# Performance work log

Hardware: AMD Instinct MI355X
Metric: run time of the kernel (lower is better)

The kernel has to match this reference:

```python
import jax, jax.numpy as jnp
import numpy as np

N_NODES = 50000
N_EDGES = 640000
HIDDEN = 128
N_LAYERS = 4
NUM_RBF = 50
CUTOFF = 4.0
N_GRAPHS = 64
VOCAB = 128
LN_EPS = 1e-5


def setup_inputs() -> dict:
    key = jax.random.key(0)
    ks = jax.random.split(key, 16)
    s = 1.0 / np.sqrt(HIDDEN)
    sr = 1.0 / np.sqrt(NUM_RBF)
    inp = {
        "x": jax.random.randint(ks[0], (N_NODES,), 0, VOCAB, dtype=jnp.int64) if jax.config.jax_enable_x64 else jax.random.randint(ks[0], (N_NODES,), 0, VOCAB).astype(jnp.int32),
        "edge_index": jax.random.randint(ks[1], (2, N_EDGES), 0, N_NODES).astype(jnp.int32),
        "edge_attr": jax.random.uniform(ks[2], (N_EDGES,), dtype=jnp.float32) * CUTOFF,
        "batch": jnp.sort(jax.random.randint(ks[3], (N_NODES,), 0, N_GRAPHS)).astype(jnp.int32),
        # embedding table
        "emb": jax.random.normal(ks[4], (VOCAB, HIDDEN), dtype=jnp.float32),
        # filter net: Linear(num_rbf, H) -> ReLU -> Linear(H, H), stacked over layers
        "fw1": jax.random.normal(ks[5], (N_LAYERS, NUM_RBF, HIDDEN), dtype=jnp.float32) * sr,
        "fb1": jnp.zeros((N_LAYERS, HIDDEN), dtype=jnp.float32),
        "fw2": jax.random.normal(ks[6], (N_LAYERS, HIDDEN, HIDDEN), dtype=jnp.float32) * s,
        "fb2": jnp.zeros((N_LAYERS, HIDDEN), dtype=jnp.float32),
        # lin: Linear(H, H) per layer
        "lw": jax.random.normal(ks[7], (N_LAYERS, HIDDEN, HIDDEN), dtype=jnp.float32) * s,
        "lb": jnp.zeros((N_LAYERS, HIDDEN), dtype=jnp.float32),
        # LayerNorm params per layer
        "ln_g": jnp.ones((N_LAYERS, HIDDEN), dtype=jnp.float32),
        "ln_b": jnp.zeros((N_LAYERS, HIDDEN), dtype=jnp.float32),
    }
    return inp


def _gaussian_smearing(dist):
    offset = jnp.linspace(0.0, CUTOFF, NUM_RBF, dtype=jnp.float32)  # [R]
    coeff = -0.5 / (CUTOFF / (NUM_RBF - 1)) ** 2
    d = dist[:, None] - offset[None, :]  # [E, R]
    return jnp.exp(coeff * d * d)


def _layer_norm(h, g, b):
    mu = jnp.mean(h, axis=-1, keepdims=True)
    var = jnp.mean(jnp.square(h - mu), axis=-1, keepdims=True)
    return (h - mu) * jax.lax.rsqrt(var + LN_EPS) * g + b


def reference(x, edge_index, edge_attr, batch, emb, fw1, fb1, fw2, fb2, lw, lb, ln_g, ln_b):
    edge_rbf = _gaussian_smearing(edge_attr)          # [E, R]
    h = emb[x]                                        # [N, H]
    row, col = edge_index[0], edge_index[1]
    for i in range(N_LAYERS):
        # FilterNet(RBF): [E, H]
        w = jax.nn.relu(edge_rbf @ fw1[i] + fb1[i]) @ fw2[i] + fb2[i]
        xl = h @ lw[i] + lb[i]                        # [N, H]
        msg = xl[col] * w                             # gather + elementwise, [E, H]
        out = jax.ops.segment_sum(msg, row, num_segments=N_NODES)
        h = _layer_norm(h + out, ln_g[i], ln_b[i])
    # global mean pool over graphs
    sums = jax.ops.segment_sum(h, batch, num_segments=N_GRAPHS)      # [G, H]
    cnt = jax.ops.segment_sum(jnp.ones((N_NODES,), h.dtype), batch, num_segments=N_GRAPHS)
    return sums / jnp.maximum(cnt, 1.0)[:, None]
```

## Files before the change

### kernel.cpp

```cpp
#include <hip/hip_runtime.h>
#include <hip/hip_bf16.h>

#define N_NODES 50000
#define N_EDGES 640000
#define HIDDEN 128
#define N_LAYERS 4
#define NUM_RBF 50
#define CUTOFF 4.0f
#define N_GRAPHS 64
#define TAB 8192
#define TG 8
#define PSPLIT 16
#define COLBITS 17
#define CMASK ((1u << COLBITS) - 1)
#define NBUCK 196
#define CHUNK 4096
#define PADMETA 990208
#define DUMMY ((uint)N_NODES)

typedef unsigned int uint;
typedef unsigned short ushort;
typedef __attribute__((ext_vector_type(8))) short bf16x8;
typedef __attribute__((ext_vector_type(4))) float f32x4;

__device__ inline ushort f2bf(float f) {
    uint u = __float_as_uint(f);
    uint r = (u + 0x7fffu + ((u >> 16) & 1u)) >> 16;
    return (ushort)r;
}
__device__ inline uint packbf(float lo, float hi) {
    return (uint)f2bf(lo) | ((uint)f2bf(hi) << 16);
}
__device__ inline float bflo(uint u) { return __uint_as_float(u << 16); }
__device__ inline float bfhi(uint u) { return __uint_as_float(u & 0xffff0000u); }

__global__ __launch_bounds__(128) void k_tab1(const float* __restrict__ fw1,
                                              const float* __restrict__ fb1,
                                              ushort* __restrict__ hidbf) {
    int bid = blockIdx.x;
    int layer = bid / (TAB / TG);
    int g0 = (bid % (TAB / TG)) * TG;
    int j = threadIdx.x;
    __shared__ float rbf[TG][NUM_RBF];
    for (int idx = j; idx < TG * NUM_RBF; idx += 128) {
        int gg = idx / NUM_RBF, r = idx % NUM_RBF;
        float d = (CUTOFF * (g0 + gg)) / (float)(TAB - 1);
        float offset = (CUTOFF * r) / (float)(NUM_RBF - 1);
        float delta = CUTOFF / (float)(NUM_RBF - 1);
        float coeff = -0.5f / (delta * delta);
        float t = d - offset;
        rbf[gg][r] = expf(coeff * t * t);
    }
    __syncthreads();
    const float* w1 = fw1 + layer * NUM_RBF * HIDDEN;
    float b1 = fb1[layer * HIDDEN + j];
    float acc[TG];
    #pragma unroll
    for (int gg = 0; gg < TG; gg++) acc[gg] = b1;
    for (int r = 0; r < NUM_RBF; r++) {
        float w = w1[r * HIDDEN + j];
        #pragma unroll
        for (int gg = 0; gg < TG; gg++) acc[gg] = fmaf(rbf[gg][r], w, acc[gg]);
    }
    #pragma unroll
    for (int gg = 0; gg < TG; gg++)
        hidbf[((size_t)layer * TAB + g0 + gg) * HIDDEN + j] = f2bf(fmaxf(acc[gg], 0.0f));
}

__global__ __launch_bounds__(256) void k_tab2(const ushort* __restrict__ hidbf,
                                              const uint4* __restrict__ pb2,
                                              const float* __restrict__ fb2,
                                              ushort* __restrict__ ctab) {
    int wave = threadIdx.x >> 6, lane = threadIdx.x & 63;
    int m0 = (blockIdx.x * 4 + wave) * 16;
    int layer = m0 / TAB;
    int quad = lane >> 4, ml = lane & 15;
    const ushort* arow = hidbf + (size_t)(m0 + ml) * HIDDEN + quad * 8;
    bf16x8 a[4];
    #pragma unroll
    for (int kc = 0; kc < 4; kc++) a[kc] = *(const bf16x8*)(arow + kc * 32);
    const uint4* pb = pb2 + (size_t)layer * 8 * 4 * 64;
    const float* bias = fb2 + layer * HIDDEN;
    #pragma unroll
    for (int nt = 0; nt < 8; nt++) {
        f32x4 acc = {0.f, 0.f, 0.f, 0.f};
        #pragma unroll
        for (int kc = 0; kc < 4; kc++) {
            bf16x8 b = *(const bf16x8*)(pb + (nt * 4 + kc) * 64 + lane);
            acc = __builtin_amdgcn_mfma_f32_16x16x32_bf16(a[kc], b, acc, 0, 0, 0);
        }
        int col = nt * 16 + ml;
        float bv = bias[col];
        #pragma unroll
        for (int r = 0; r < 4; r++) {
            int row = m0 + quad * 4 + r;
            ctab[(size_t)row * HIDDEN + col] = f2bf(acc[r] + bv);
        }
    }
}

__global__ void k_embed(const int* __restrict__ x, const float* __restrict__ emb,
                        ushort* __restrict__ hbf) {
    int idx = blockIdx.x * 256 + threadIdx.x;
    if (idx >= N_NODES * 32) return;
    int n = idx >> 5, q = idx & 31;
    float4 v = ((const float4*)emb)[x[n] * 32 + q];
    uint2 p;
    p.x = packbf(v.x, v.y);
    p.y = packbf(v.z, v.w);
    ((uint2*)hbf)[idx] = p;
}

__global__ void k_packw(const float* __restrict__ lw, const float* __restrict__ fw2,
                        uint4* __restrict__ pb, uint4* __restrict__ pb2) {
    int idx = blockIdx.x * 256 + threadIdx.x;
    if (idx >= 2 * N_LAYERS * 8 * 4 * 64) return;
    int which = idx >> 13;
    int rem = idx & 8191;
    int lane = rem & 63;
    int kc = (rem >> 6) & 3;
    int nt = (rem >> 8) & 7;
    int layer = rem >> 11;
    int quad = lane >> 4, nl = lane & 15;
    int n = nt * 16 + nl;
    const float* w = (which ? fw2 : lw) + layer * HIDDEN * HIDDEN;
    uint r[4];
    #pragma unroll
    for (int jj = 0; jj < 4; jj++) {
        int k = kc * 32 + quad * 8 + 2 * jj;
        r[jj] = packbf(w[k * HIDDEN + n], w[(k + 1) * HIDDEN + n]);
    }
    uint4 o; o.x = r[0]; o.y = r[1]; o.z = r[2]; o.w = r[3];
    (which ? pb2 : pb)[rem] = o;
}

__global__ void k_count(const int* __restrict__ row, int* __restrict__ counts) {
    int e = blockIdx.x * 256 + threadIdx.x;
    if (e < N_EDGES) atomicAdd(&counts[row[e]], 1);
}

__global__ void k_scan1(const int* __restrict__ counts, int* __restrict__ partial,
                        int* __restrict__ blocksum) {
    int i = blockIdx.x * 256 + threadIdx.x;
    int c = (i < N_NODES) ? counts[i] : 0;
    int v = (c + 7) & ~7;
    int lane = threadIdx.x & 63;
    int wid = threadIdx.x >> 6;
    int s = v;
    #pragma unroll
    for (int off = 1; off < 64; off <<= 1) {
        int t = __shfl_up(s, off, 64);
        if (lane >= off) s += t;
    }
    __shared__ int wsum[4];
    if (lane == 63) wsum[wid] = s;
    __syncthreads();
    int woff = 0;
    for (int w = 0; w < wid; w++) woff += wsum[w];
    int incl = s + woff;
    if (i < N_NODES) partial[i] = incl - v;
    if (threadIdx.x == 255) blocksum[blockIdx.x] = incl;
}

__global__ void k_scan2(int* __restrict__ blocksum, int nblk,
                        const int* __restrict__ batch, int* __restrict__ gstart,
                        int* __restrict__ padtotal) {
    int tid = threadIdx.x;
    if (tid <= N_GRAPHS) {
        int lo = 0, hi = N_NODES;
        while (lo < hi) {
            int mid = (lo + hi) >> 1;
            if (batch[mid] < tid) lo = mid + 1; else hi = mid;
        }
        gstart[tid] = lo;
    }
    int v = (tid < nblk) ? blocksum[tid] : 0;
    int lane = tid & 63, wid = tid >> 6;
    int s = v;
    #pragma unroll
    for (int off = 1; off < 64; off <<= 1) {
        int t = __shfl_up(s, off, 64);
        if (lane >= off) s += t;
    }
    __shared__ int wsum[4];
    if (lane == 63) wsum[wid] = s;
    __syncthreads();
    int woff = 0;
    for (int w = 0; w < wid; w++) woff += wsum[w];
    int incl = s + woff;
    if (tid < nblk) blocksum[tid] = incl - v;
    if (tid == nblk - 1) *padtotal = incl;
}

__global__ void k_scan3(const int* __restrict__ partial, const int* __restrict__ blocksum,
                        const int* __restrict__ padtotal,
                        int* __restrict__ offsets, int* __restrict__ bcur) {
    int i = blockIdx.x * 256 + threadIdx.x;
    if (i < N_NODES) {
        int o = partial[i] + blocksum[blockIdx.x];
        offsets[i] = o;
        if ((i & 255) == 0) bcur[i >> 8] = o;
    }
    if (i == 0) offsets[N_NODES] = *padtotal;
}

__global__ __launch_bounds__(256) void k_bucket(const int* __restrict__ row,
                                                const int* __restrict__ col,
                                                const float* __restrict__ eattr,
                                                int* __restrict__ bcur,
                                                uint2* __restrict__ bs) {
    __shared__ uint2 stage[CHUNK];
    __shared__ int hist[256], lscan[256], lcur[256], gbase[256];
    __shared__ int wsum[4];
    int t = threadIdx.x;
    int e0 = blockIdx.x * CHUNK;
    int ne = min(CHUNK, N_EDGES - e0);
    hist[t] = 0;
    __syncthreads();
    for (int i = t; i < ne; i += 256)
        atomicAdd(&hist[row[e0 + i] >> 8], 1);
    __syncthreads();
    int v = hist[t];
    int lane = t & 63, wid = t >> 6;
    int s = v;
    #pragma unroll
    for (int off = 1; off < 64; off <<= 1) {
        int u = __shfl_up(s, off, 64);
        if (lane >= off) s += u;
    }
    if (lane == 63) wsum[wid] = s;
    __syncthreads();
    int woff = 0;
    for (int w = 0; w < wid; w++) woff += wsum[w];
    int excl = s + woff - v;
    lscan[t] = excl;
    lcur[t] = excl;
    if (v > 0) gbase[t] = atomicAdd(&bcur[t], v);
    __syncthreads();
    for (int i = t; i < ne; i += 256) {
        int e = e0 + i;
        int r = row[e];
        float tt = eattr[e] * ((float)(TAB - 1) / CUTOFF);
        int gi = (int)(tt + 0.5f);
        gi = min(max(gi, 0), TAB - 1);
        int pos = atomicAdd(&lcur[r >> 8], 1);
        uint2 sv;
        sv.x = (uint)col[e] | ((uint)gi << COLBITS);
        sv.y = (uint)r;
        stage[pos] = sv;
    }
    __syncthreads();
    for (int i = t; i < ne; i += 256) {
        uint2 sv = stage[i];
        int b = sv.y >> 8;
        bs[gbase[b] + (i - lscan[b])] = sv;
    }
}

__global__ __launch_bounds__(256) void k_scatter(const uint2* __restrict__ bs,
                                                 const int* __restrict__ offsets,
                                                 const int* __restrict__ bend,
                                                 uint* __restrict__ meta) {
    int b = blockIdx.x, t = threadIdx.x;
    int r0 = b << 8;
    __shared__ int cur[256];
    int rmax = min(r0 + 256, N_NODES);
    cur[t] = offsets[min(r0 + t, N_NODES)];
    __syncthreads();
    int s = offsets[r0], e = bend[b];
    for (int i = s + t; i < e; i += 256) {
        uint2 v = bs[i];
        int slot = atomicAdd(&cur[v.y - r0], 1);
        meta[slot] = v.x;
    }
    __syncthreads();
    int node = r0 + t;
    if (node < rmax) {
        int end = offsets[node + 1];
        for (int i = cur[t]; i < end; i++) meta[i] = DUMMY;
    }
}

__global__ __launch_bounds__(256) void k_xl(const ushort* __restrict__ hbf,
                                            const uint4* __restrict__ pb,
                                            const float* __restrict__ lb,
                                            ushort* __restrict__ xlb) {
    int wave = threadIdx.x >> 6, lane = threadIdx.x & 63;
    int m0 = (blockIdx.x * 4 + wave) * 16;
    if (m0 >= N_NODES) return;
    int quad = lane >> 4, ml = lane & 15;
    const ushort* arow = hbf + (size_t)(m0 + ml) * HIDDEN + quad * 8;
    bf16x8 a[4];
    #pragma unroll
    for (int kc = 0; kc < 4; kc++) a[kc] = *(const bf16x8*)(arow + kc * 32);
    #pragma unroll
    for (int nt = 0; nt < 8; nt++) {
        f32x4 acc = {0.f, 0.f, 0.f, 0.f};
        #pragma unroll
        for (int kc = 0; kc < 4; kc++) {
            bf16x8 b = *(const bf16x8*)(pb + (nt * 4 + kc) * 64 + lane);
            acc = __builtin_amdgcn_mfma_f32_16x16x32_bf16(a[kc], b, acc, 0, 0, 0);
        }
        int col = nt * 16 + ml;
        float bias = lb[col];
        #pragma unroll
        for (int r = 0; r < 4; r++) {
            int row = m0 + quad * 4 + r;
            xlb[(size_t)row * HIDDEN + col] = f2bf(acc[r] + bias);
        }
    }
}

__global__ __launch_bounds__(256) void k_agg(const ushort* __restrict__ xlb,
                                             const uint* __restrict__ meta,
                                             const int* __restrict__ offsets,
                                             const uint* __restrict__ ctab,
                                             const ushort* __restrict__ hb_in,
                                             const float* __restrict__ g,
                                             const float* __restrict__ b,
                                             ushort* __restrict__ hbf_out) {
    int wid = threadIdx.x >> 6;
    int lane = threadIdx.x & 63;
    int n = blockIdx.x * 4 + wid;
    if (n >= N_NODES) return;
    const uint* xl2 = (const uint*)xlb;
    float accx = 0.f, accy = 0.f;
    int p0 = offsets[n], p1 = offsets[n + 1];
    int cnt = p1 - p0;
    for (int base = 0; base < cnt; base += 64) {
        int li = p0 + base + lane;
        uint mlv = meta[min(li, PADMETA - 1)];
        int kk = min(64, cnt - base);
        int p = 0;
        for (; p + 16 <= kk; p += 16) {
            uint wA[8], xA[8], wB[8], xB[8];
            #pragma unroll
            for (int i = 0; i < 8; i++) {
                uint m = __builtin_amdgcn_readlane(mlv, p + i);
                wA[i] = ctab[(m >> COLBITS) * 64 + lane];
                xA[i] = xl2[(m & CMASK) * 64 + lane];
            }
            #pragma unroll
            for (int i = 0; i < 8; i++) {
                uint m = __builtin_amdgcn_readlane(mlv, p + 8 + i);
                wB[i] = ctab[(m >> COLBITS) * 64 + lane];
                xB[i] = xl2[(m & CMASK) * 64 + lane];
            }
            #pragma unroll
            for (int i = 0; i < 8; i++) {
                accx = fmaf(bflo(wA[i]), bflo(xA[i]), accx);
                accy = fmaf(bfhi(wA[i]), bfhi(xA[i]), accy);
            }
            #pragma unroll
            for (int i = 0; i < 8; i++) {
                accx = fmaf(bflo(wB[i]), bflo(xB[i]), accx);
                accy = fmaf(bfhi(wB[i]), bfhi(xB[i]), accy);
            }
        }
        for (; p < kk; p += 8) {
            uint wA[8], xA[8];
            #pragma unroll
            for (int i = 0; i < 8; i++) {
                uint m = __builtin_amdgcn_readlane(mlv, p + i);
                wA[i] = ctab[(m >> COLBITS) * 64 + lane];
                xA[i] = xl2[(m & CMASK) * 64 + lane];
            }
            #pragma unroll
            for (int i = 0; i < 8; i++) {
                accx = fmaf(bflo(wA[i]), bflo(xA[i]), accx);
                accy = fmaf(bfhi(wA[i]), bfhi(xA[i]), accy);
            }
        }
    }
    uint hvp = ((const uint*)hb_in)[n * 64 + lane];
    float vx = bflo(hvp) + accx, vy = bfhi(hvp) + accy;
    float s = vx + vy;
    #pragma unroll
    for (int off = 32; off; off >>= 1) s += __shfl_xor(s, off, 64);
    float mu = s * (1.0f / 128.0f);
    float dx = vx - mu, dy = vy - mu;
    float s2 = dx * dx + dy * dy;
    #pragma unroll
    for (int off = 32; off; off >>= 1) s2 += __shfl_xor(s2, off, 64);
    float rstd = rsqrtf(s2 * (1.0f / 128.0f) + 1e-5f);
    float2 gv = ((const float2*)g)[lane];
    float2 bv = ((const float2*)b)[lane];
    float ox = fmaf(dx * rstd, gv.x, bv.x);
    float oy = fmaf(dy * rstd, gv.y, bv.y);
    ((uint*)hbf_out)[n * 64 + lane] = packbf(ox, oy);
}

__global__ __launch_bounds__(256) void k_pool_part(const ushort* __restrict__ hbf,
                                                   const int* __restrict__ gstart,
                                                   float* __restrict__ partial) {
    int g = blockIdx.x / PSPLIT;
    int t = blockIdx.x % PSPLIT;
    int jp = threadIdx.x & 63;
    int half = threadIdx.x >> 6;
    int s = gstart[g], e = gstart[g + 1];
    float accx = 0.f, accy = 0.f;
    const uint* h2 = (const uint*)hbf;
    for (int n = s + t * 4 + half; n < e; n += PSPLIT * 4) {
        uint v = h2[n * 64 + jp];
        accx += bflo(v);
        accy += bfhi(v);
    }
    __shared__ float redx[256], redy[256];
    redx[threadIdx.x] = accx;
    redy[threadIdx.x] = accy;
    __syncthreads();
    if (half == 0) {
        float tx = redx[jp] + redx[jp + 64] + redx[jp + 128] + redx[jp + 192];
        float ty = redy[jp] + redy[jp + 64] + redy[jp + 128] + redy[jp + 192];
        float2 o; o.x = tx; o.y = ty;
        ((float2*)partial)[(g * PSPLIT + t) * 64 + jp] = o;
    }
}

__global__ void k_pool_fin(const float* __restrict__ partial,
                           const int* __restrict__ gstart,
                           float* __restrict__ out) {
    int idx = blockIdx.x * 128 + threadIdx.x;
    int g = idx >> 7, j = idx & 127;
    float tot = 0.f;
    #pragma unroll
    for (int t = 0; t < PSPLIT; t++) tot += partial[(g * PSPLIT + t) * HIDDEN + j];
    float c = (float)(gstart[g + 1] - gstart[g]);
    out[idx] = tot / fmaxf(c, 1.0f);
}

extern "C" void kernel_launch(void* const* d_in, const int* in_sizes, int n_in,
                              void* d_out, int out_size, void* d_ws, size_t ws_size,
                              hipStream_t stream) {
    const int* x = (const int*)d_in[0];
    const int* edge_index = (const int*)d_in[1];
    const int* row = edge_index;
    const int* col = edge_index + N_EDGES;
    const float* eattr = (const float*)d_in[2];
    const int* batch = (const int*)d_in[3];
    const float* emb = (const float*)d_in[4];
    const float* fw1 = (const float*)d_in[5];
    const float* fb1 = (const float*)d_in[6];
    const float* fw2 = (const float*)d_in[7];
    const float* fb2 = (const float*)d_in[8];
    const float* lw = (const float*)d_in[9];
    const float* lb = (const float*)d_in[10];
    const float* ln_g = (const float*)d_in[11];
    const float* ln_b = (const float*)d_in[12];
    float* out = (float*)d_out;

    char* ws = (char*)d_ws;
    size_t off = 0;
    auto alloc = [&](size_t bytes) -> void* {
        void* p = ws + off;
        off = (off + bytes + 255) & ~(size_t)255;
        return p;
    };
    uint* ctab     = (uint*)alloc((size_t)N_LAYERS * TAB * 64 * 4);
    ushort* hidbf  = (ushort*)alloc((size_t)N_LAYERS * TAB * HIDDEN * 2);
    ushort* hbf_a  = (ushort*)alloc((size_t)N_NODES * HIDDEN * 2);
    ushort* hbf_b  = (ushort*)alloc((size_t)N_NODES * HIDDEN * 2);
    ushort* xlb    = (ushort*)alloc((size_t)(N_NODES + 1) * HIDDEN * 2);
    uint4* pb      = (uint4*)alloc((size_t)N_LAYERS * 8 * 4 * 64 * 16);
    uint4* pb2     = (uint4*)alloc((size_t)N_LAYERS * 8 * 4 * 64 * 16);
    int* counts    = (int*)alloc((size_t)(N_NODES + 1) * 4);
    int* offsets   = (int*)alloc((size_t)(N_NODES + 1) * 4);
    int* partial   = (int*)alloc((size_t)N_NODES * 4);
    int* blocksum  = (int*)alloc(256 * 4);
    int* bcur      = (int*)alloc(256 * 4);
    int* padtotal  = (int*)alloc(256);
    uint2* bs      = (uint2*)alloc((size_t)PADMETA * 8);
    uint* meta     = (uint*)alloc((size_t)PADMETA * 4);
    int* gstart    = (int*)alloc((size_t)(N_GRAPHS + 1) * 4);
    float* ppart   = (float*)alloc((size_t)N_GRAPHS * PSPLIT * HIDDEN * 4);

    hipMemsetAsync(counts, 0, (size_t)(N_NODES + 1) * 4, stream);
    hipMemsetAsync(xlb + (size_t)N_NODES * HIDDEN, 0, HIDDEN * 2, stream);

    k_packw<<<(2 * N_LAYERS * 8 * 4 * 64 + 255) / 256, 256, 0, stream>>>(lw, fw2, pb, pb2);
    k_tab1<<<N_LAYERS * (TAB / TG), 128, 0, stream>>>(fw1, fb1, hidbf);
    k_tab2<<<(N_LAYERS * TAB) / 64, 256, 0, stream>>>(hidbf, pb2, fb2, (ushort*)ctab);
    k_embed<<<(N_NODES * 32 + 255) / 256, 256, 0, stream>>>(x, emb, hbf_a);
    k_count<<<(N_EDGES + 255) / 256, 256, 0, stream>>>(row, counts);
    const int NBLK = (N_NODES + 255) / 256;
    k_scan1<<<NBLK, 256, 0, stream>>>(counts, partial, blocksum);
    k_scan2<<<1, 256, 0, stream>>>(blocksum, NBLK, batch, gstart, padtotal);
    k_scan3<<<NBLK, 256, 0, stream>>>(partial, blocksum, padtotal, offsets, bcur);
    k_bucket<<<(N_EDGES + CHUNK - 1) / CHUNK, 256, 0, stream>>>(row, col, eattr, bcur, bs);
    k_scatter<<<NBUCK, 256, 0, stream>>>(bs, offsets, bcur, meta);

    ushort* hb_cur = hbf_a; ushort* hb_nxt = hbf_b;
    const int XLBLK = (N_NODES / 16 + 3) / 4;
    for (int i = 0; i < N_LAYERS; i++) {
        k_xl<<<XLBLK, 256, 0, stream>>>(hb_cur, pb + (size_t)i * 8 * 4 * 64,
                                        lb + i * HIDDEN, xlb);
        k_agg<<<(N_NODES + 3) / 4, 256, 0, stream>>>(xlb, meta, offsets,
                                                     ctab + (size_t)i * TAB * 64,
                                                     hb_cur, ln_g + i * HIDDEN,
                                                     ln_b + i * HIDDEN, hb_nxt);
        ushort* tb = hb_cur; hb_cur = hb_nxt; hb_nxt = tb;
    }
    k_pool_part<<<N_GRAPHS * PSPLIT, 256, 0, stream>>>(hb_cur, gstart, ppart);
    k_pool_fin<<<(N_GRAPHS * HIDDEN + 127) / 128, 128, 0, stream>>>(ppart, gstart, out);
}
```

Before: 371.5 us.

## Merge preprocessing kernels and fuse filter-table stages through shared memory

Combines weight packing, embedding lookup, degree counting and the dummy-row zeroing into one multi-role kernel. It fuses the two filter-table kernels so the hidden activations stay in LDS instead of making a global round trip. It also replaces the three-kernel scan with a single 1024-thread block that loops over tiles. The goal is fewer launches and less global traffic, at the cost of a serial single-block scan over 49 tiles and higher register use in the table kernel.

```diff
diff --git a/kernel.cpp b/kernel.cpp
--- a/kernel.cpp
+++ b/kernel.cpp
@@ -9,7 +9,6 @@
 #define CUTOFF 4.0f
 #define N_GRAPHS 64
 #define TAB 8192
-#define TG 8
 #define PSPLIT 16
 #define COLBITS 17
 #define CMASK ((1u << COLBITS) - 1)
@@ -18,6 +17,10 @@
 #define PADMETA 990208
 #define DUMMY ((uint)N_NODES)
 
+#define PB_PACKW 64
+#define PB_EMBED 6250
+#define PB_COUNT 2500
+
 typedef unsigned int uint;
 typedef unsigned short ushort;
 typedef __attribute__((ext_vector_type(8))) short bf16x8;
@@ -34,174 +37,161 @@
 __device__ inline float bflo(uint u) { return __uint_as_float(u << 16); }
 __device__ inline float bfhi(uint u) { return __uint_as_float(u & 0xffff0000u); }
 
-__global__ __launch_bounds__(128) void k_tab1(const float* __restrict__ fw1,
-                                              const float* __restrict__ fb1,
-                                              ushort* __restrict__ hidbf) {
-    int bid = blockIdx.x;
-    int layer = bid / (TAB / TG);
-    int g0 = (bid % (TAB / TG)) * TG;
-    int j = threadIdx.x;
-    __shared__ float rbf[TG][NUM_RBF];
-    for (int idx = j; idx < TG * NUM_RBF; idx += 128) {
+__global__ __launch_bounds__(256) void k_prep(const float* __restrict__ lw,
+                                              const float* __restrict__ fw2,
+                                              uint4* __restrict__ pb,
+                                              uint4* __restrict__ pb2,
+                                              const int* __restrict__ x,
+                                              const float* __restrict__ emb,
+                                              ushort* __restrict__ hbf,
+                                              const int* __restrict__ row,
+                                              int* __restrict__ counts,
+                                              ushort* __restrict__ xlb) {
+    int b = blockIdx.x, t = threadIdx.x;
+    if (b < PB_PACKW) {
+        int idx = b * 256 + t;
+        int which = idx >> 13;
+        int rem = idx & 8191;
+        int lane = rem & 63;
+        int kc = (rem >> 6) & 3;
+        int nt = (rem >> 8) & 7;
+        int layer = rem >> 11;
+        int quad = lane >> 4, nl = lane & 15;
+        int n = nt * 16 + nl;
+        const float* w = (which ? fw2 : lw) + layer * HIDDEN * HIDDEN;
+        uint r[4];
+        #pragma unroll
+        for (int jj = 0; jj < 4; jj++) {
+            int k = kc * 32 + quad * 8 + 2 * jj;
+            r[jj] = packbf(w[k * HIDDEN + n], w[(k + 1) * HIDDEN + n]);
+        }
+        uint4 o; o.x = r[0]; o.y = r[1]; o.z = r[2]; o.w = r[3];
+        (which ? pb2 : pb)[rem] = o;
+    } else if (b < PB_PACKW + PB_EMBED) {
+        int idx = (b - PB_PACKW) * 256 + t;
+        if (idx < N_NODES * 32) {
+            int n = idx >> 5, q = idx & 31;
+            float4 v = ((const float4*)emb)[x[n] * 32 + q];
+            uint2 p;
+            p.x = packbf(v.x, v.y);
+            p.y = packbf(v.z, v.w);
+            ((uint2*)hbf)[idx] = p;
+        }
+    } else if (b < PB_PACKW + PB_EMBED + PB_COUNT) {
+        int e = (b - PB_PACKW - PB_EMBED) * 256 + t;
+        if (e < N_EDGES) atomicAdd(&counts[row[e]], 1);
+    } else {
+        if (t < 64) ((uint*)(xlb + (size_t)N_NODES * HIDDEN))[t] = 0;
+    }
+}
+
+__global__ __launch_bounds__(256) void k_tab(const float* __restrict__ fw1,
+                                             const float* __restrict__ fb1,
+                                             const uint4* __restrict__ pb2,
+                                             const float* __restrict__ fb2,
+                                             ushort* __restrict__ ctab) {
+    int layer = blockIdx.x / (TAB / 64);
+    int g0 = (blockIdx.x % (TAB / 64)) * 64;
+    int t = threadIdx.x;
+    __shared__ float rbf[64][NUM_RBF];
+    __shared__ ushort hid[64][HIDDEN];
+    for (int idx = t; idx < 64 * NUM_RBF; idx += 256) {
         int gg = idx / NUM_RBF, r = idx % NUM_RBF;
         float d = (CUTOFF * (g0 + gg)) / (float)(TAB - 1);
         float offset = (CUTOFF * r) / (float)(NUM_RBF - 1);
         float delta = CUTOFF / (float)(NUM_RBF - 1);
         float coeff = -0.5f / (delta * delta);
-        float t = d - offset;
-        rbf[gg][r] = expf(coeff * t * t);
-    }
-    __syncthreads();
-    const float* w1 = fw1 + layer * NUM_RBF * HIDDEN;
-    float b1 = fb1[layer * HIDDEN + j];
-    float acc[TG];
-    #pragma unroll
-    for (int gg = 0; gg < TG; gg++) acc[gg] = b1;
-    for (int r = 0; r < NUM_RBF; r++) {
-        float w = w1[r * HIDDEN + j];
-        #pragma unroll
-        for (int gg = 0; gg < TG; gg++) acc[gg] = fmaf(rbf[gg][r], w, acc[gg]);
-    }
-    #pragma unroll
-    for (int gg = 0; gg < TG; gg++)
-        hidbf[((size_t)layer * TAB + g0 + gg) * HIDDEN + j] = f2bf(fmaxf(acc[gg], 0.0f));
-}
-
-__global__ __launch_bounds__(256) void k_tab2(const ushort* __restrict__ hidbf,
-                                              const uint4* __restrict__ pb2,
-                                              const float* __restrict__ fb2,
-                                              ushort* __restrict__ ctab) {
-    int wave = threadIdx.x >> 6, lane = threadIdx.x & 63;
-    int m0 = (blockIdx.x * 4 + wave) * 16;
-    int layer = m0 / TAB;
+        float tt = d - offset;
+        rbf[gg][r] = expf(coeff * tt * tt);
+    }
+    __syncthreads();
+    {
+        int ch = t & 127;
+        int gb = (t >> 7) * 32;
+        const float* w1 = fw1 + layer * NUM_RBF * HIDDEN;
+        float b1 = fb1[layer * HIDDEN + ch];
+        float acc[32];
+        #pragma unroll
+        for (int i = 0; i < 32; i++) acc[i] = b1;
+        for (int r = 0; r < NUM_RBF; r++) {
+            float w = w1[r * HIDDEN + ch];
+            #pragma unroll
+            for (int i = 0; i < 32; i++) acc[i] = fmaf(rbf[gb + i][r], w, acc[i]);
+        }
+        #pragma unroll
+        for (int i = 0; i < 32; i++) hid[gb + i][ch] = f2bf(fmaxf(acc[i], 0.0f));
+    }
+    __syncthreads();
+    int wave = t >> 6, lane = t & 63;
     int quad = lane >> 4, ml = lane & 15;
-    const ushort* arow = hidbf + (size_t)(m0 + ml) * HIDDEN + quad * 8;
+    const ushort* arow = &hid[wave * 16 + ml][quad * 8];
     bf16x8 a[4];
     #pragma unroll
     for (int kc = 0; kc < 4; kc++) a[kc] = *(const bf16x8*)(arow + kc * 32);
     const uint4* pb = pb2 + (size_t)layer * 8 * 4 * 64;
     const float* bias = fb2 + layer * HIDDEN;
+    int m0 = layer * TAB + g0 + wave * 16;
     #pragma unroll
     for (int nt = 0; nt < 8; nt++) {
         f32x4 acc = {0.f, 0.f, 0.f, 0.f};
         #pragma unroll
         for (int kc = 0; kc < 4; kc++) {
-            bf16x8 b = *(const bf16x8*)(pb + (nt * 4 + kc) * 64 + lane);
-            acc = __builtin_amdgcn_mfma_f32_16x16x32_bf16(a[kc], b, acc, 0, 0, 0);
+            bf16x8 bfr = *(const bf16x8*)(pb + (nt * 4 + kc) * 64 + lane);
+            acc = __builtin_amdgcn_mfma_f32_16x16x32_bf16(a[kc], bfr, acc, 0, 0, 0);
         }
         int col = nt * 16 + ml;
         float bv = bias[col];
         #pragma unroll
         for (int r = 0; r < 4; r++) {
-            int row = m0 + quad * 4 + r;
-            ctab[(size_t)row * HIDDEN + col] = f2bf(acc[r] + bv);
-        }
-    }
-}
-
-__global__ void k_embed(const int* __restrict__ x, const float* __restrict__ emb,
-                        ushort* __restrict__ hbf) {
-    int idx = blockIdx.x * 256 + threadIdx.x;
-    if (idx >= N_NODES * 32) return;
-    int n = idx >> 5, q = idx & 31;
-    float4 v = ((const float4*)emb)[x[n] * 32 + q];
-    uint2 p;
-    p.x = packbf(v.x, v.y);
-    p.y = packbf(v.z, v.w);
-    ((uint2*)hbf)[idx] = p;
-}
-
-__global__ void k_packw(const float* __restrict__ lw, const float* __restrict__ fw2,
-                        uint4* __restrict__ pb, uint4* __restrict__ pb2) {
-    int idx = blockIdx.x * 256 + threadIdx.x;
-    if (idx >= 2 * N_LAYERS * 8 * 4 * 64) return;
-    int which = idx >> 13;
-    int rem = idx & 8191;
-    int lane = rem & 63;
-    int kc = (rem >> 6) & 3;
-    int nt = (rem >> 8) & 7;
-    int layer = rem >> 11;
-    int quad = lane >> 4, nl = lane & 15;
-    int n = nt * 16 + nl;
-    const float* w = (which ? fw2 : lw) + layer * HIDDEN * HIDDEN;
-    uint r[4];
-    #pragma unroll
-    for (int jj = 0; jj < 4; jj++) {
-        int k = kc * 32 + quad * 8 + 2 * jj;
-        r[jj] = packbf(w[k * HIDDEN + n], w[(k + 1) * HIDDEN + n]);
-    }
-    uint4 o; o.x = r[0]; o.y = r[1]; o.z = r[2]; o.w = r[3];
-    (which ? pb2 : pb)[rem] = o;
-}
-
-__global__ void k_count(const int* __restrict__ row, int* __restrict__ counts) {
-    int e = blockIdx.x * 256 + threadIdx.x;
-    if (e < N_EDGES) atomicAdd(&counts[row[e]], 1);
-}
-
-__global__ void k_scan1(const int* __restrict__ counts, int* __restrict__ partial,
-                        int* __restrict__ blocksum) {
-    int i = blockIdx.x * 256 + threadIdx.x;
-    int c = (i < N_NODES) ? counts[i] : 0;
-    int v = (c + 7) & ~7;
-    int lane = threadIdx.x & 63;
-    int wid = threadIdx.x >> 6;
-    int s = v;
-    #pragma unroll
-    for (int off = 1; off < 64; off <<= 1) {
-        int t = __shfl_up(s, off, 64);
-        if (lane >= off) s += t;
-    }
-    __shared__ int wsum[4];
-    if (lane == 63) wsum[wid] = s;
-    __syncthreads();
-    int woff = 0;
-    for (int w = 0; w < wid; w++) woff += wsum[w];
-    int incl = s + woff;
-    if (i < N_NODES) partial[i] = incl - v;
-    if (threadIdx.x == 255) blocksum[blockIdx.x] = incl;
-}
-
-__global__ void k_scan2(int* __restrict__ blocksum, int nblk,
-                        const int* __restrict__ batch, int* __restrict__ gstart,
-                        int* __restrict__ padtotal) {
-    int tid = threadIdx.x;
-    if (tid <= N_GRAPHS) {
+            int rowi = m0 + quad * 4 + r;
+            ctab[(size_t)rowi * HIDDEN + col] = f2bf(acc[r] + bv);
+        }
+    }
+}
+
+__global__ __launch_bounds__(1024) void k_scanall(const int* __restrict__ counts,
+                                                  int* __restrict__ offsets,
+                                                  int* __restrict__ bcur,
+                                                  const int* __restrict__ batch,
+                                                  int* __restrict__ gstart) {
+    int t = threadIdx.x;
+    int lane = t & 63, wv = t >> 6;
+    __shared__ int wsum[16];
+    __shared__ int carry;
+    if (t == 0) carry = 0;
+    __syncthreads();
+    const int NT = (N_NODES + 1023) / 1024;
+    for (int tile = 0; tile < NT; tile++) {
+        int i = tile * 1024 + t;
+        int v = (i < N_NODES) ? ((counts[i] + 7) & ~7) : 0;
+        int s = v;
+        #pragma unroll
+        for (int off = 1; off < 64; off <<= 1) {
+            int u = __shfl_up(s, off, 64);
+            if (lane >= off) s += u;
+        }
+        if (lane == 63) wsum[wv] = s;
+        __syncthreads();
+        int woff = 0;
+        for (int w = 0; w < wv; w++) woff += wsum[w];
+        int excl = s + woff - v + carry;
+        if (i < N_NODES) {
+            offsets[i] = excl;
+            if ((i & 255) == 0) bcur[i >> 8] = excl;
+        }
+        __syncthreads();
+        if (t == 1023) carry = excl + v;
+        __syncthreads();
+    }
+    if (t == 0) offsets[N_NODES] = carry;
+    if (t <= N_GRAPHS) {
         int lo = 0, hi = N_NODES;
         while (lo < hi) {
             int mid = (lo + hi) >> 1;
-            if (batch[mid] < tid) lo = mid + 1; else hi = mid;
-        }
-        gstart[tid] = lo;
-    }
-    int v = (tid < nblk) ? blocksum[tid] : 0;
-    int lane = tid & 63, wid = tid >> 6;
-    int s = v;
-    #pragma unroll
-    for (int off = 1; off < 64; off <<= 1) {
-        int t = __shfl_up(s, off, 64);
-        if (lane >= off) s += t;
-    }
-    __shared__ int wsum[4];
-    if (lane == 63) wsum[wid] = s;
-    __syncthreads();
-    int woff = 0;
-    for (int w = 0; w < wid; w++) woff += wsum[w];
-    int incl = s + woff;
-    if (tid < nblk) blocksum[tid] = incl - v;
-    if (tid == nblk - 1) *padtotal = incl;
-}
-
-__global__ void k_scan3(const int* __restrict__ partial, const int* __restrict__ blocksum,
-                        const int* __restrict__ padtotal,
-                        int* __restrict__ offsets, int* __restrict__ bcur) {
-    int i = blockIdx.x * 256 + threadIdx.x;
-    if (i < N_NODES) {
-        int o = partial[i] + blocksum[blockIdx.x];
-        offsets[i] = o;
-        if ((i & 255) == 0) bcur[i >> 8] = o;
-    }
-    if (i == 0) offsets[N_NODES] = *padtotal;
+            if (batch[mid] < t) lo = mid + 1; else hi = mid;
+        }
+        gstart[t] = lo;
+    }
 }
 
 __global__ __launch_bounds__(256) void k_bucket(const int* __restrict__ row,
@@ -457,7 +447,6 @@
         return p;
     };
     uint* ctab     = (uint*)alloc((size_t)N_LAYERS * TAB * 64 * 4);
-    ushort* hidbf  = (ushort*)alloc((size_t)N_LAYERS * TAB * HIDDEN * 2);
     ushort* hbf_a  = (ushort*)alloc((size_t)N_NODES * HIDDEN * 2);
     ushort* hbf_b  = (ushort*)alloc((size_t)N_NODES * HIDDEN * 2);
     ushort* xlb    = (ushort*)alloc((size_t)(N_NODES + 1) * HIDDEN * 2);
@@ -465,27 +454,19 @@
     uint4* pb2     = (uint4*)alloc((size_t)N_LAYERS * 8 * 4 * 64 * 16);
     int* counts    = (int*)alloc((size_t)(N_NODES + 1) * 4);
     int* offsets   = (int*)alloc((size_t)(N_NODES + 1) * 4);
-    int* partial   = (int*)alloc((size_t)N_NODES * 4);
-    int* blocksum  = (int*)alloc(256 * 4);
     int* bcur      = (int*)alloc(256 * 4);
-    int* padtotal  = (int*)alloc(256);
     uint2* bs      = (uint2*)alloc((size_t)PADMETA * 8);
     uint* meta     = (uint*)alloc((size_t)PADMETA * 4);
     int* gstart    = (int*)alloc((size_t)(N_GRAPHS + 1) * 4);
     float* ppart   = (float*)alloc((size_t)N_GRAPHS * PSPLIT * HIDDEN * 4);
 
     hipMemsetAsync(counts, 0, (size_t)(N_NODES + 1) * 4, stream);
-    hipMemsetAsync(xlb + (size_t)N_NODES * HIDDEN, 0, HIDDEN * 2, stream);
-
-    k_packw<<<(2 * N_LAYERS * 8 * 4 * 64 + 255) / 256, 256, 0, stream>>>(lw, fw2, pb, pb2);
-    k_tab1<<<N_LAYERS * (TAB / TG), 128, 0, stream>>>(fw1, fb1, hidbf);
-    k_tab2<<<(N_LAYERS * TAB) / 64, 256, 0, stream>>>(hidbf, pb2, fb2, (ushort*)ctab);
-    k_embed<<<(N_NODES * 32 + 255) / 256, 256, 0, stream>>>(x, emb, hbf_a);
-    k_count<<<(N_EDGES + 255) / 256, 256, 0, stream>>>(row, counts);
-    const int NBLK = (N_NODES + 255) / 256;
-    k_scan1<<<NBLK, 256, 0, stream>>>(counts, partial, blocksum);
-    k_scan2<<<1, 256, 0, stream>>>(blocksum, NBLK, batch, gstart, padtotal);
-    k_scan3<<<NBLK, 256, 0, stream>>>(partial, blocksum, padtotal, offsets, bcur);
+
+    const int PREP_GRID = PB_PACKW + PB_EMBED + PB_COUNT + 1;
+    k_prep<<<PREP_GRID, 256, 0, stream>>>(lw, fw2, pb, pb2, x, emb, hbf_a,
+                                          row, counts, xlb);
+    k_tab<<<N_LAYERS * (TAB / 64), 256, 0, stream>>>(fw1, fb1, pb2, fb2, (ushort*)ctab);
+    k_scanall<<<1, 1024, 0, stream>>>(counts, offsets, bcur, batch, gstart);
     k_bucket<<<(N_EDGES + CHUNK - 1) / CHUNK, 256, 0, stream>>>(row, col, eattr, bcur, bs);
     k_scatter<<<NBUCK, 256, 0, stream>>>(bs, offsets, bcur, meta);
 
```

Result: slower. 416.6 us (+12.1%).
